# Optimization experiments

Measured on AMD Instinct MI355X. Metric: run time of the kernel, lower is better.

Reference implementation:

```python
import jax, jax.numpy as jnp
import numpy as np

N, E, F, ED, L = 50000, 800000, 64, 16, 2
EPS_BN = 1e-5


def setup_inputs() -> dict:
    key = jax.random.key(0)
    ks = jax.random.split(key, 8)
    s = 0.05
    return {
        "x": jax.random.normal(ks[0], (N, F), jnp.float32),
        "edge_index": jax.random.randint(ks[1], (2, E), 0, N),
        "edge_attr": jax.random.normal(ks[2], (E, ED), jnp.float32),
        # per-layer stacked params (L layers)
        "We": jax.random.normal(ks[3], (L, ED, F), jnp.float32) * s,
        "be": jnp.zeros((L, F), jnp.float32),
        "Wpre": jax.random.normal(ks[4], (L, 2 * F, F), jnp.float32) * s,
        "bpre": jnp.zeros((L, F), jnp.float32),
        "Wpost": jax.random.normal(ks[5], (L, 7 * F, F), jnp.float32) * s,
        "bpost": jnp.zeros((L, F), jnp.float32),
        "Wlin": jax.random.normal(ks[6], (L, F, F), jnp.float32) * s,
        "blin": jnp.zeros((L, F), jnp.float32),
        "gamma": jnp.ones((L, F), jnp.float32),
        "beta": jnp.zeros((L, F), jnp.float32),
    }


def _layer(x, src, dst, edge_attr, We, be, Wpre, bpre, Wpost, bpost, Wlin, blin, gamma, beta):
    # message: edge encoder + pre-MLP on cat(x_j, e)   [E, F]
    e = edge_attr @ We + be
    h = jnp.concatenate([x[src], e], axis=-1) @ Wpre + bpre
    # multi-aggregator segment reduce to target nodes (index = dst)
    cnt = jax.ops.segment_sum(jnp.ones(h.shape[0], h.dtype), dst, num_segments=N)
    safe_cnt = jnp.maximum(cnt, 1.0)
    mean = jax.ops.segment_sum(h, dst, num_segments=N) / safe_cnt[:, None]
    empty = (cnt == 0)[:, None]
    mn = jnp.where(empty, 0.0, jax.ops.segment_min(h, dst, num_segments=N))
    mx = jnp.where(empty, 0.0, jax.ops.segment_max(h, dst, num_segments=N))
    agg = jnp.concatenate([mean, mn, mx], axis=-1)  # [N, 3F]
    # scalers: identity, then amplification (deg=None => avg from bincount of degrees)
    deg_i = cnt.astype(jnp.int32)
    bc = jnp.bincount(deg_i, length=N).astype(h.dtype)
    avg_log = jnp.mean(jnp.log(bc + 1.0))
    amp = (jnp.log(safe_cnt + 1.0) / avg_log)[:, None]
    out = jnp.concatenate([agg, agg * amp], axis=-1)  # [N, 6F]
    # post-MLP on cat(x, aggregated), final linear
    out = jnp.concatenate([x, out], axis=-1) @ Wpost + bpost  # [N, F]
    out = out @ Wlin + blin
    # BatchNorm1d (batch stats, biased var) + ReLU
    mu = out.mean(axis=0)
    var = jnp.mean((out - mu) ** 2, axis=0)
    out = gamma * (out - mu) / jnp.sqrt(var + EPS_BN) + beta
    return jax.nn.relu(out)


def reference(x, edge_index, edge_attr, We, be, Wpre, bpre, Wpost, bpost, Wlin, blin, gamma, beta):
    src, dst = edge_index[0], edge_index[1]
    for l in range(L):
        x = _layer(x, src, dst, edge_attr, We[l], be[l], Wpre[l], bpre[l],
                   Wpost[l], bpost[l], Wlin[l], blin[l], gamma[l], beta[l])
    return x
```

## Files before the change

### kernel.cpp

```cpp
#include <hip/hip_runtime.h>
#include <math.h>

static constexpr int NN = 50000;
static constexpr long NE = 800000;
static constexpr int FF = 64;
static constexpr int EDIM = 16;
static constexpr int NLAYER = 2;
static constexpr float EPSBN = 1e-5f;
static constexpr int NGRP = NN / 16;
static constexpr int SCB = 512;
static constexpr int NSCB = (NN + SCB - 1) / SCB;
static constexpr int LDSW = 68;

typedef __attribute__((ext_vector_type(8))) short short8v;
typedef __attribute__((ext_vector_type(4))) float f32x4;

#define MFMA16(a, b, c) __builtin_amdgcn_mfma_f32_16x16x32_bf16(a, b, c, 0, 0, 0)

__device__ __forceinline__ short f2bf(float f) {
    unsigned u = __float_as_uint(f);
    unsigned r = u + 0x7FFFu + ((u >> 16) & 1u);
    return (short)(r >> 16);
}
__device__ __forceinline__ float bf2f(unsigned short h) {
    return __uint_as_float(((unsigned)h) << 16);
}
__device__ __forceinline__ unsigned pk2(float lo, float hi) {
    return (unsigned)(unsigned short)f2bf(lo) | ((unsigned)(unsigned short)f2bf(hi) << 16);
}
__device__ __forceinline__ short8v pack8(const float* p) {
    const float4* q = (const float4*)p;
    float4 a = q[0], b = q[1];
    short8v v;
    v[0] = f2bf(a.x); v[1] = f2bf(a.y); v[2] = f2bf(a.z); v[3] = f2bf(a.w);
    v[4] = f2bf(b.x); v[5] = f2bf(b.y); v[6] = f2bf(b.z); v[7] = f2bf(b.w);
    return v;
}
__device__ __forceinline__ void pack8s(const float* p, short8v& hi, short8v& lo) {
    const float4* q = (const float4*)p;
    float4 a = q[0], b = q[1];
    float v[8] = {a.x, a.y, a.z, a.w, b.x, b.y, b.z, b.w};
#pragma unroll
    for (int j = 0; j < 8; ++j) {
        short h = f2bf(v[j]);
        hi[j] = h;
        lo[j] = f2bf(v[j] - bf2f((unsigned short)h));
    }
}
__device__ __forceinline__ void pack8fs(const float* v, short8v& hi, short8v& lo) {
#pragma unroll
    for (int j = 0; j < 8; ++j) {
        short h = f2bf(v[j]);
        hi[j] = h;
        lo[j] = f2bf(v[j] - bf2f((unsigned short)h));
    }
}

__global__ void fold_kernel(const float* __restrict__ We, const float* __restrict__ be,
                            const float* __restrict__ Wpre, const float* __restrict__ bpre,
                            const float* __restrict__ Wpost, const float* __restrict__ bpost,
                            const float* __restrict__ Wlin, const float* __restrict__ blin,
                            float* __restrict__ Weff, float* __restrict__ beff,
                            float* __restrict__ Wc, float* __restrict__ cfold) {
    int l = blockIdx.x >> 4;
    int s = blockIdx.x & 15;
    int t = threadIdx.x;
    const float* We_l    = We    + l * EDIM * FF;
    const float* Wpre_e  = Wpre  + l * 2 * FF * FF + FF * FF;
    const float* Wpost_l = Wpost + l * 7 * FF * FF;
    const float* Wlin_l  = Wlin  + l * FF * FF;

    __shared__ float slin[FF * FF];
    __shared__ float spre[FF * FF];
    for (int i = t; i < FF * FF; i += blockDim.x) { slin[i] = Wlin_l[i]; spre[i] = Wpre_e[i]; }
    __syncthreads();

    for (int i = s * 256 + t; i < EDIM * FF; i += 16 * 256) {
        int j = i >> 6, f = i & 63;
        float a = 0.f;
        for (int k = 0; k < FF; ++k) a += We_l[j * FF + k] * spre[k * FF + f];
        Weff[l * EDIM * FF + i] = a;
    }
    for (int i = s * 256 + t; i < FF; i += 16 * 256) {
        float a = bpre[l * FF + i];
        for (int k = 0; k < FF; ++k) a += be[l * FF + k] * spre[k * FF + i];
        beff[l * FF + i] = a;
    }
    for (int i = s * 256 + t; i < 7 * FF * FF; i += 16 * 256) {
        int r = i >> 6, f = i & 63;
        float a = 0.f;
        for (int k = 0; k < FF; ++k) a += Wpost_l[r * FF + k] * slin[k * FF + f];
        Wc[l * 7 * FF * FF + i] = a;
    }
    for (int i = s * 256 + t; i < FF; i += 16 * 256) {
        float a = blin[l * FF + i];
        for (int k = 0; k < FF; ++k) a += bpost[l * FF + k] * slin[k * FF + i];
        cfold[l * FF + i] = a;
    }
}

__global__ void fragify_all(const float* __restrict__ Wpre, const float* __restrict__ Weff,
                            const float* __restrict__ Wc,
                            short* __restrict__ WpreF, short* __restrict__ WeffF,
                            short* __restrict__ WcFh, short* __restrict__ WcFl) {
    int b = blockIdx.x;
    int l = b / 17, r = b % 17;
    int t = threadIdx.x;
    const float* src; short* dh; short* dl = nullptr; int kc, Kreal;
    if (r < 2)      { src = Wpre + (size_t)l * 2 * FF * FF; dh = WpreF + l * 4096;  kc = r;     Kreal = 64; }
    else if (r < 3) { src = Weff + (size_t)l * EDIM * FF;   dh = WeffF + l * 2048;  kc = 0;     Kreal = 16; }
    else            { src = Wc   + (size_t)l * 7 * FF * FF; dh = WcFh + l * 28672;
                      dl = WcFl + l * 28672;                                        kc = r - 3; Kreal = 448; }
    int idx = kc * 256 + t;
    int lane = idx & 63, nt = (idx >> 6) & 3;
    int m = lane & 15, kh = lane >> 4;
    short8v hv, lv;
#pragma unroll
    for (int j = 0; j < 8; ++j) {
        int k = kc * 32 + kh * 8 + j;
        float val = (k < Kreal) ? src[k * FF + nt * 16 + m] : 0.f;
        short h = f2bf(val);
        hv[j] = h;
        lv[j] = f2bf(val - bf2f((unsigned short)h));
    }
    ((short8v*)dh)[idx] = hv;
    if (dl) ((short8v*)dl)[idx] = lv;
}


__global__ void build_zero(int* __restrict__ rowcnt, int* __restrict__ fill,
                           int* __restrict__ bc, float* __restrict__ avglog) {
    long i = (long)blockIdx.x * 256 + threadIdx.x;
    long stride = (long)gridDim.x * 256;
    for (long j = i; j < NN; j += stride) { rowcnt[j] = 0; fill[j] = 0; bc[j] = 0; }
    if (i == 0) avglog[0] = 0.f;
}

__global__ void hist_dst(const int* __restrict__ ei, int* __restrict__ rowcnt) {
    long e = (long)blockIdx.x * 256 + threadIdx.x;
    if (e < NE) atomicAdd(&rowcnt[ei[NE + e]], 1);
}

__global__ void scan_a(const int* __restrict__ rowcnt, int* __restrict__ part) {
    __shared__ int red[SCB];
    int t = threadIdx.x;
    int i = blockIdx.x * SCB + t;
    red[t] = (i < NN) ? rowcnt[i] : 0;
    __syncthreads();
    for (int o = SCB / 2; o > 0; o >>= 1) {
        if (t < o) red[t] += red[t + o];
        __syncthreads();
    }
    if (t == 0) part[blockIdx.x] = red[0];
}

__global__ void scan_b(int* __restrict__ part, int* __restrict__ rowptr) {
    __shared__ int s[128];
    int t = threadIdx.x;
    int v = (t < NSCB) ? part[t] : 0;
    s[t] = v;
    __syncthreads();
    for (int o = 1; o < 128; o <<= 1) {
        int u = (t >= o) ? s[t - o] : 0;
        __syncthreads();
        s[t] += u;
        __syncthreads();
    }
    if (t < NSCB) part[t] = s[t] - v;
    if (t == 127) rowptr[NN] = s[127];
}

__global__ void scan_c(const int* __restrict__ rowcnt, const int* __restrict__ part,
                       int* __restrict__ rowptr) {
    __shared__ int s[SCB];
    int t = threadIdx.x;
    int i = blockIdx.x * SCB + t;
    int v = (i < NN) ? rowcnt[i] : 0;
    s[t] = v;
    __syncthreads();
    for (int o = 1; o < SCB; o <<= 1) {
        int u = (t >= o) ? s[t - o] : 0;
        __syncthreads();
        s[t] += u;
        __syncthreads();
    }
    if (i < NN) rowptr[i] = part[blockIdx.x] + s[t] - v;
}

__global__ void scatter_perm(const int* __restrict__ ei, const int* __restrict__ rowptr,
                             int* __restrict__ fill, int2* __restrict__ srcperm) {
    long e = (long)blockIdx.x * 256 + threadIdx.x;
    if (e >= NE) return;
    int d = ei[NE + e];
    int p = rowptr[d] + atomicAdd(&fill[d], 1);
    srcperm[p] = make_int2(ei[e], (int)e);
}

__global__ void gather_attr(const int2* __restrict__ srcperm, const float* __restrict__ attr,
                            int* __restrict__ srcp, short* __restrict__ attrb) {
    long p = (long)blockIdx.x * 256 + threadIdx.x;
    if (p >= NE) return;
    int2 sp = srcperm[p];
    srcp[p] = sp.x;
    long e = sp.y;
    const float4* a4 = (const float4*)(attr + e * EDIM);
    float4 A = a4[0], B = a4[1], C = a4[2], D = a4[3];
    uint4 w0, w1;
    w0.x = pk2(A.x, A.y); w0.y = pk2(A.z, A.w); w0.z = pk2(B.x, B.y); w0.w = pk2(B.z, B.w);
    w1.x = pk2(C.x, C.y); w1.y = pk2(C.z, C.w); w1.z = pk2(D.x, D.y); w1.w = pk2(D.z, D.w);
    uint4* dst = (uint4*)(attrb + p * EDIM);
    dst[0] = w0; dst[1] = w1;
}

__global__ void degbc2(const int* __restrict__ rowcnt, int* __restrict__ bc) {
    __shared__ int h[256];
    int t = threadIdx.x;
    h[t] = 0;
    __syncthreads();
    for (long n = (long)blockIdx.x * 256 + t; n < NN; n += (long)gridDim.x * 256) {
        int d = rowcnt[n];
        if (d < 256) {
            atomicAdd(&h[d], 1);
        } else {
            if (d >= NN) d = NN - 1;
            atomicAdd(&bc[d], 1);
        }
    }
    __syncthreads();
    int v = h[t];
    if (v) atomicAdd(&bc[t], v);
}

__global__ void avglog_kernel(const int* __restrict__ bc, float* __restrict__ total) {
    float s = 0.f;
    for (long i = (long)blockIdx.x * 256 + threadIdx.x; i < NN; i += (long)gridDim.x * 256)
        s += logf((float)bc[i] + 1.f);
    for (int o = 32; o; o >>= 1) s += __shfl_down(s, o, 64);
    __shared__ float wsum[4];
    int lane = threadIdx.x & 63, wid = threadIdx.x >> 6;
    if (lane == 0) wsum[wid] = s;
    __syncthreads();
    if (threadIdx.x == 0) atomicAdd(total, wsum[0] + wsum[1] + wsum[2] + wsum[3]);
}

__global__ void amp_kernel(const int* __restrict__ cnt, const float* __restrict__ total,
                           float* __restrict__ amp) {
    long n = (long)blockIdx.x * 256 + threadIdx.x;
    if (n < NN) {
        float avg = total[0] / (float)NN;
        float sc = fmaxf((float)cnt[n], 1.f);
        amp[n] = logf(sc + 1.f) / avg;
    }
}


__global__ __launch_bounds__(256) void xp_mfma(const float* __restrict__ xin,
                                               const short* __restrict__ WF,
                                               short* __restrict__ xpb,
                                               float* __restrict__ bnsum,
                                               float* __restrict__ bnsum2) {
    int t = threadIdx.x;
    if (blockIdx.x == 0 && t < FF) { bnsum[t] = 0.f; bnsum2[t] = 0.f; }
    int g = blockIdx.x * 4 + (t >> 6);
    if (g >= NGRP) return;
    int lane = t & 63, m = lane & 15, kh = lane >> 4;
    const float* xr = xin + (long)(g * 16 + m) * FF;
    short8v a0 = pack8(xr + kh * 8);
    short8v a1 = pack8(xr + 32 + kh * 8);
    const short8v* BF = (const short8v*)WF;
    f32x4 acc[4];
#pragma unroll
    for (int nt = 0; nt < 4; ++nt) {
        f32x4 z = {0.f, 0.f, 0.f, 0.f};
        z = MFMA16(a0, BF[(0 * 4 + nt) * 64 + lane], z);
        z = MFMA16(a1, BF[(1 * 4 + nt) * 64 + lane], z);
        acc[nt] = z;
    }
#pragma unroll
    for (int nt = 0; nt < 4; ++nt)
#pragma unroll
        for (int r = 0; r < 4; ++r) {
            long node = g * 16 + kh * 4 + r;
            xpb[node * FF + nt * 16 + m] = f2bf(acc[nt][r]);
        }
}

__global__ __launch_bounds__(256) void agg_fused(
    const int* __restrict__ rowptr, const int* __restrict__ srcp,
    const short* __restrict__ attrb, const short* __restrict__ WF,
    const float* __restrict__ beff_l, const short* __restrict__ xpb,
    float* __restrict__ sumb, float* __restrict__ mnb, float* __restrict__ mxb) {
    __shared__ float eph[4][16 * LDSW];
    int t = threadIdx.x;
    int wid = t >> 6, lane = t & 63;
    int m = lane & 15, kh = lane >> 4;
    int n = blockIdx.x * 4 + wid;
    if (n >= NN) return;
    float* lds = &eph[wid][0];
    const short8v* BF = (const short8v*)WF;
    float bfv[4];
#pragma unroll
    for (int nt = 0; nt < 4; ++nt) bfv[nt] = beff_l[nt * 16 + m];
    long r0 = rowptr[n], r1 = rowptr[n + 1];
    const float INF = __builtin_huge_valf();
    float sm = 0.f, mn = INF, mx = -INF;
    const unsigned short* xu = (const unsigned short*)xpb;

    for (long base = r0; base < r1; base += 16) {
        int cnt = (int)(((r1 - base) < 16) ? (r1 - base) : 16);
        long ea = base + m; if (ea > NE - 1) ea = NE - 1;
        short8v a;
        if (kh < 2) {
            a = *(const short8v*)(attrb + ea * EDIM + kh * 8);
        } else {
#pragma unroll
            for (int j = 0; j < 8; ++j) a[j] = 0;
        }
        f32x4 ac0, ac1, ac2, ac3;
        {
            f32x4 z = {0.f, 0.f, 0.f, 0.f};
            ac0 = MFMA16(a, BF[0 * 64 + lane], z);
            ac1 = MFMA16(a, BF[1 * 64 + lane], z);
            ac2 = MFMA16(a, BF[2 * 64 + lane], z);
            ac3 = MFMA16(a, BF[3 * 64 + lane], z);
        }
#pragma unroll
        for (int r = 0; r < 4; ++r) {
            lds[(kh * 4 + r) * LDSW + 0 * 16 + m] = ac0[r] + bfv[0];
            lds[(kh * 4 + r) * LDSW + 1 * 16 + m] = ac1[r] + bfv[1];
            lds[(kh * 4 + r) * LDSW + 2 * 16 + m] = ac2[r] + bfv[2];
            lds[(kh * 4 + r) * LDSW + 3 * 16 + m] = ac3[r] + bfv[3];
        }
        int sv = srcp[base + (lane < cnt ? lane : cnt - 1)];
        int j = 0;
        for (; j + 8 <= cnt; j += 8) {
            int s0 = __shfl(sv, j + 0), s1 = __shfl(sv, j + 1);
            int s2 = __shfl(sv, j + 2), s3 = __shfl(sv, j + 3);
            int s4 = __shfl(sv, j + 4), s5 = __shfl(sv, j + 5);
            int s6 = __shfl(sv, j + 6), s7 = __shfl(sv, j + 7);
            float x0 = bf2f(xu[(long)s0 * FF + lane]);
            float x1 = bf2f(xu[(long)s1 * FF + lane]);
            float x2 = bf2f(xu[(long)s2 * FF + lane]);
            float x3 = bf2f(xu[(long)s3 * FF + lane]);
            float x4 = bf2f(xu[(long)s4 * FF + lane]);
            float x5 = bf2f(xu[(long)s5 * FF + lane]);
            float x6 = bf2f(xu[(long)s6 * FF + lane]);
            float x7 = bf2f(xu[(long)s7 * FF + lane]);
            float h0 = x0 + lds[(j + 0) * LDSW + lane];
            float h1 = x1 + lds[(j + 1) * LDSW + lane];
            float h2 = x2 + lds[(j + 2) * LDSW + lane];
            float h3 = x3 + lds[(j + 3) * LDSW + lane];
            float h4 = x4 + lds[(j + 4) * LDSW + lane];
            float h5 = x5 + lds[(j + 5) * LDSW + lane];
            float h6 = x6 + lds[(j + 6) * LDSW + lane];
            float h7 = x7 + lds[(j + 7) * LDSW + lane];
            sm += ((h0 + h1) + (h2 + h3)) + ((h4 + h5) + (h6 + h7));
            mn = fminf(mn, fminf(fminf(fminf(h0, h1), fminf(h2, h3)),
                                 fminf(fminf(h4, h5), fminf(h6, h7))));
            mx = fmaxf(mx, fmaxf(fmaxf(fmaxf(h0, h1), fmaxf(h2, h3)),
                                 fmaxf(fmaxf(h4, h5), fmaxf(h6, h7))));
        }
        for (; j < cnt; ++j) {
            int s0 = __shfl(sv, j);
            float h = bf2f(xu[(long)s0 * FF + lane]) + lds[j * LDSW + lane];
            sm += h;
            mn = fminf(mn, h);
            mx = fmaxf(mx, h);
        }
    }
    long o = (long)n * FF + lane;
    sumb[o] = sm; mnb[o] = mn; mxb[o] = mx;
}

__global__ __launch_bounds__(256) void node_mfma(
    const float* __restrict__ xin, const float* __restrict__ sumb,
    const float* __restrict__ mnb, const float* __restrict__ mxb,
    const int* __restrict__ rowcnt, const float* __restrict__ amp,
    const short* __restrict__ WFh, const short* __restrict__ WFl,
    const float* __restrict__ cfold_l,
    float* __restrict__ out_pre, float* __restrict__ bnsum, float* __restrict__ bnsum2) {
    __shared__ float sS[FF], sQ[FF];
    int t = threadIdx.x;
    if (t < FF) { sS[t] = 0.f; sQ[t] = 0.f; }
    __syncthreads();
    int g = blockIdx.x * 4 + (t >> 6);
    bool act = (g < NGRP);
    int lane = t & 63, m = lane & 15, kh = lane >> 4;
    if (act) {
        long n = g * 16 + m;
        int deg = rowcnt[n];
        float inv = 1.f / fmaxf((float)deg, 1.f);
        bool has = (deg > 0);
        float av = amp[n];
        const float* xr = xin + n * FF;
        float vme[16], vmn[16], vmx[16], sc16[16];
        {
            const float4* s4a = (const float4*)(sumb + n * FF + kh * 8);
            const float4* s4b = (const float4*)(sumb + n * FF + 32 + kh * 8);
            float4 a = s4a[0], b = s4a[1], c = s4b[0], d = s4b[1];
            vme[0]=a.x*inv; vme[1]=a.y*inv; vme[2]=a.z*inv; vme[3]=a.w*inv;
            vme[4]=b.x*inv; vme[5]=b.y*inv; vme[6]=b.z*inv; vme[7]=b.w*inv;
            vme[8]=c.x*inv; vme[9]=c.y*inv; vme[10]=c.z*inv; vme[11]=c.w*inv;
            vme[12]=d.x*inv; vme[13]=d.y*inv; vme[14]=d.z*inv; vme[15]=d.w*inv;
        }
        {
            const float4* s4a = (const float4*)(mnb + n * FF + kh * 8);
            const float4* s4b = (const float4*)(mnb + n * FF + 32 + kh * 8);
            float4 a = s4a[0], b = s4a[1], c = s4b[0], d = s4b[1];
            vmn[0]=has?a.x:0.f; vmn[1]=has?a.y:0.f; vmn[2]=has?a.z:0.f; vmn[3]=has?a.w:0.f;
            vmn[4]=has?b.x:0.f; vmn[5]=has?b.y:0.f; vmn[6]=has?b.z:0.f; vmn[7]=has?b.w:0.f;
            vmn[8]=has?c.x:0.f; vmn[9]=has?c.y:0.f; vmn[10]=has?c.z:0.f; vmn[11]=has?c.w:0.f;
            vmn[12]=has?d.x:0.f; vmn[13]=has?d.y:0.f; vmn[14]=has?d.z:0.f; vmn[15]=has?d.w:0.f;
        }
        {
            const float4* s4a = (const float4*)(mxb + n * FF + kh * 8);
            const float4* s4b = (const float4*)(mxb + n * FF + 32 + kh * 8);
            float4 a = s4a[0], b = s4a[1], c = s4b[0], d = s4b[1];
            vmx[0]=has?a.x:0.f; vmx[1]=has?a.y:0.f; vmx[2]=has?a.z:0.f; vmx[3]=has?a.w:0.f;
            vmx[4]=has?b.x:0.f; vmx[5]=has?b.y:0.f; vmx[6]=has?b.z:0.f; vmx[7]=has?b.w:0.f;
            vmx[8]=has?c.x:0.f; vmx[9]=has?c.y:0.f; vmx[10]=has?c.z:0.f; vmx[11]=has?c.w:0.f;
            vmx[12]=has?d.x:0.f; vmx[13]=has?d.y:0.f; vmx[14]=has?d.z:0.f; vmx[15]=has?d.w:0.f;
        }
        const short8v* BH = (const short8v*)WFh;
        const short8v* BL = (const short8v*)WFl;
        f32x4 acc[4];
#pragma unroll
        for (int nt = 0; nt < 4; ++nt) { f32x4 z = {0.f,0.f,0.f,0.f}; acc[nt] = z; }
        short8v hv, lv;
#define DO_KC3(kc) { \
        _Pragma("unroll") for (int nt = 0; nt < 4; ++nt) { \
            acc[nt] = MFMA16(hv, BH[((kc) * 4 + nt) * 64 + lane], acc[nt]); \
            acc[nt] = MFMA16(lv, BH[((kc) * 4 + nt) * 64 + lane], acc[nt]); \
            acc[nt] = MFMA16(hv, BL[((kc) * 4 + nt) * 64 + lane], acc[nt]); } }
        pack8s(xr + kh * 8, hv, lv);        DO_KC3(0)
        pack8s(xr + 32 + kh * 8, hv, lv);   DO_KC3(1)
        pack8fs(vme + 0, hv, lv);           DO_KC3(2)
        pack8fs(vme + 8, hv, lv);           DO_KC3(3)
        pack8fs(vmn + 0, hv, lv);           DO_KC3(4)
        pack8fs(vmn + 8, hv, lv);           DO_KC3(5)
        pack8fs(vmx + 0, hv, lv);           DO_KC3(6)
        pack8fs(vmx + 8, hv, lv);           DO_KC3(7)
#pragma unroll
        for (int j = 0; j < 16; ++j) sc16[j] = vme[j] * av;
        pack8fs(sc16 + 0, hv, lv);          DO_KC3(8)
        pack8fs(sc16 + 8, hv, lv);          DO_KC3(9)
#pragma unroll
        for (int j = 0; j < 16; ++j) sc16[j] = vmn[j] * av;
        pack8fs(sc16 + 0, hv, lv);          DO_KC3(10)
        pack8fs(sc16 + 8, hv, lv);          DO_KC3(11)
#pragma unroll
        for (int j = 0; j < 16; ++j) sc16[j] = vmx[j] * av;
        pack8fs(sc16 + 0, hv, lv);          DO_KC3(12)
        pack8fs(sc16 + 8, hv, lv);          DO_KC3(13)
#undef DO_KC3
        float cfv[4];
#pragma unroll
        for (int nt = 0; nt < 4; ++nt) cfv[nt] = cfold_l[nt * 16 + m];
#pragma unroll
        for (int nt = 0; nt < 4; ++nt) {
            float ps = 0.f, pq = 0.f;
#pragma unroll
            for (int r = 0; r < 4; ++r) {
                float v = acc[nt][r] + cfv[nt];
                out_pre[(long)(g * 16 + kh * 4 + r) * FF + nt * 16 + m] = v;
                ps += v;
                pq += v * v;
            }
            atomicAdd(&sS[nt * 16 + m], ps);
            atomicAdd(&sQ[nt * 16 + m], pq);
        }
    }
    __syncthreads();
    if (t < FF) {
        atomicAdd(&bnsum[t], sS[t]);
        atomicAdd(&bnsum2[t], sQ[t]);
    }
}

__global__ void bn_apply2(const float* __restrict__ out_pre,
                          const float* __restrict__ bnsum, const float* __restrict__ bnsum2,
                          const float* __restrict__ gamma_l, const float* __restrict__ beta_l,
                          float* __restrict__ xout) {
    int f = threadIdx.x & 63;
    float mu = bnsum[f] / (float)NN;
    float var = bnsum2[f] / (float)NN - mu * mu;
    var = fmaxf(var, 0.f);
    float s = gamma_l[f] * rsqrtf(var + EPSBN);
    float o = beta_l[f] - mu * s;
    long i = (long)blockIdx.x * 256 + threadIdx.x;
    long stride = (long)gridDim.x * 256;
    for (long j = i; j < (long)NN * FF; j += stride) {
        xout[j] = fmaxf(fmaf(out_pre[j], s, o), 0.f);
    }
}

extern "C" void kernel_launch(void* const* d_in, const int* in_sizes, int n_in,
                              void* d_out, int out_size, void* d_ws, size_t ws_size,
                              hipStream_t stream) {
    const float* x0    = (const float*)d_in[0];
    const int*   ei    = (const int*)d_in[1];
    const float* attr  = (const float*)d_in[2];
    const float* We    = (const float*)d_in[3];
    const float* be    = (const float*)d_in[4];
    const float* Wpre  = (const float*)d_in[5];
    const float* bpre  = (const float*)d_in[6];
    const float* Wpost = (const float*)d_in[7];
    const float* bpost = (const float*)d_in[8];
    const float* Wlin  = (const float*)d_in[9];
    const float* blin  = (const float*)d_in[10];
    const float* gamma = (const float*)d_in[11];
    const float* beta  = (const float*)d_in[12];
    float* out = (float*)d_out;

    char* ws = (char*)d_ws;
    size_t off = 0;
    auto carve = [&](size_t bytes) -> void* {
        void* p = ws + off;
        off += (bytes + 255) & ~(size_t)255;
        return p;
    };
    const size_t NFb = (size_t)NN * FF * 4;
    float*    Weff   = (float*)carve(2 * EDIM * FF * 4);
    float*    beff   = (float*)carve(2 * FF * 4);
    float*    Wc     = (float*)carve(2 * 7 * FF * FF * 4);
    float*    cfold  = (float*)carve(2 * FF * 4);
    short*    WpreF  = (short*)carve(2 * 4096 * 2);
    short*    WeffF  = (short*)carve(2 * 2048 * 2);
    short*    WcFh   = (short*)carve(2 * 28672 * 2);
    short*    WcFl   = (short*)carve(2 * 28672 * 2);
    int*      srcp   = (int*)carve(NE * 4);
    short*    attrb  = (short*)carve((size_t)NE * EDIM * 2);
    int*      rowptr = (int*)carve((NN + 1) * 4);
    int*      rowcnt = (int*)carve(NN * 4);
    int*      fill   = (int*)carve(NN * 4);
    int*      bc     = (int*)carve(NN * 4);
    float*    amp    = (float*)carve(NN * 4);
    int*      part   = (int*)carve(NSCB * 4);
    short*    xpb    = (short*)carve((size_t)NN * FF * 2);
    float*    sumb   = (float*)carve(NFb);
    float*    mnb    = (float*)carve(NFb);
    float*    mxb    = (float*)carve(NFb);
    float*    xbuf   = (float*)carve(NFb);
    float*    out_pre = (float*)carve(NFb);
    float*    bnsum  = (float*)carve(FF * 4);
    float*    bnsum2 = (float*)carve(FF * 4);
    float*    avglog = (float*)carve(4);
    int2*     srcperm = (int2*)xbuf;

    const int EB = (int)((NE + 255) / 256);

    build_zero<<<196, 256, 0, stream>>>(rowcnt, fill, bc, avglog);
    hist_dst<<<EB, 256, 0, stream>>>(ei, rowcnt);
    scan_a<<<NSCB, SCB, 0, stream>>>(rowcnt, part);
    scan_b<<<1, 128, 0, stream>>>(part, rowptr);
    scan_c<<<NSCB, SCB, 0, stream>>>(rowcnt, part, rowptr);
    scatter_perm<<<EB, 256, 0, stream>>>(ei, rowptr, fill, srcperm);
    gather_attr<<<EB, 256, 0, stream>>>(srcperm, attr, srcp, attrb);
    degbc2<<<196, 256, 0, stream>>>(rowcnt, bc);
    avglog_kernel<<<128, 256, 0, stream>>>(bc, avglog);
    amp_kernel<<<196, 256, 0, stream>>>(rowcnt, avglog, amp);
    fold_kernel<<<32, 256, 0, stream>>>(We, be, Wpre, bpre, Wpost, bpost, Wlin, blin,
                                        Weff, beff, Wc, cfold);
    fragify_all<<<34, 256, 0, stream>>>(Wpre, Weff, Wc, WpreF, WeffF, WcFh, WcFl);

    for (int l = 0; l < NLAYER; ++l) {
        const float* xin = (l == 0) ? x0 : xbuf;
        float* xout = (l == NLAYER - 1) ? out : xbuf;

        xp_mfma<<<(NGRP + 3) / 4, 256, 0, stream>>>(xin, WpreF + l * 4096, xpb, bnsum, bnsum2);
        agg_fused<<<12500, 256, 0, stream>>>(rowptr, srcp, attrb, WeffF + l * 2048,
                                             beff + l * FF, xpb, sumb, mnb, mxb);
        node_mfma<<<(NGRP + 3) / 4, 256, 0, stream>>>(xin, sumb, mnb, mxb, rowcnt, amp,
                                                      WcFh + l * 28672, WcFl + l * 28672,
                                                      cfold + l * FF,
                                                      out_pre, bnsum, bnsum2);
        bn_apply2<<<4096, 256, 0, stream>>>(out_pre, bnsum, bnsum2,
                                            gamma + l * FF, beta + l * FF, xout);
    }
}
```

Baseline: 348.5 us.

## Fuse BatchNorm+ReLU of inner layer into next layer's input loads

For every layer except the last, the separate BN-apply pass is replaced by a tiny kernel that computes per-feature scale and shift. The next layer's xp_mfma and node_mfma apply scale, shift and ReLU while loading the raw pre-activations. This removes a full N×F read and write pass per inner layer, but the affine transform is now computed twice, once in each consumer. The diff also moves mean division and empty-node zeroing into agg_fused, splits the node_mfma accumulators into two independent chains, and adds a launch_bounds occupancy hint.

```diff
diff --git a/kernel.cpp b/kernel.cpp
--- a/kernel.cpp
+++ b/kernel.cpp
@@ -36,6 +36,18 @@
     v[4] = f2bf(b.x); v[5] = f2bf(b.y); v[6] = f2bf(b.z); v[7] = f2bf(b.w);
     return v;
 }
+__device__ __forceinline__ short8v pack8bn(const float* p, const float* sc, int f0) {
+    const float4* q = (const float4*)p;
+    float4 a = q[0], b = q[1];
+    float v[8] = {a.x, a.y, a.z, a.w, b.x, b.y, b.z, b.w};
+    short8v r;
+#pragma unroll
+    for (int j = 0; j < 8; ++j) {
+        float y = fmaxf(fmaf(v[j], sc[f0 + j], sc[FF + f0 + j]), 0.f);
+        r[j] = f2bf(y);
+    }
+    return r;
+}
 __device__ __forceinline__ void pack8s(const float* p, short8v& hi, short8v& lo) {
     const float4* q = (const float4*)p;
     float4 a = q[0], b = q[1];
@@ -45,6 +57,19 @@
         short h = f2bf(v[j]);
         hi[j] = h;
         lo[j] = f2bf(v[j] - bf2f((unsigned short)h));
+    }
+}
+__device__ __forceinline__ void pack8s_bn(const float* p, const float* sc, int f0,
+                                          short8v& hi, short8v& lo) {
+    const float4* q = (const float4*)p;
+    float4 a = q[0], b = q[1];
+    float v[8] = {a.x, a.y, a.z, a.w, b.x, b.y, b.z, b.w};
+#pragma unroll
+    for (int j = 0; j < 8; ++j) {
+        float y = fmaxf(fmaf(v[j], sc[f0 + j], sc[FF + f0 + j]), 0.f);
+        short h = f2bf(y);
+        hi[j] = h;
+        lo[j] = f2bf(y - bf2f((unsigned short)h));
     }
 }
 __device__ __forceinline__ void pack8fs(const float* v, short8v& hi, short8v& lo) {
@@ -255,6 +280,7 @@
 
 
 __global__ __launch_bounds__(256) void xp_mfma(const float* __restrict__ xin,
+                                               const float* __restrict__ bnsc,
                                                const short* __restrict__ WF,
                                                short* __restrict__ xpb,
                                                float* __restrict__ bnsum,
@@ -265,8 +291,14 @@
     if (g >= NGRP) return;
     int lane = t & 63, m = lane & 15, kh = lane >> 4;
     const float* xr = xin + (long)(g * 16 + m) * FF;
-    short8v a0 = pack8(xr + kh * 8);
-    short8v a1 = pack8(xr + 32 + kh * 8);
+    short8v a0, a1;
+    if (bnsc) {
+        a0 = pack8bn(xr + kh * 8, bnsc, kh * 8);
+        a1 = pack8bn(xr + 32 + kh * 8, bnsc, 32 + kh * 8);
+    } else {
+        a0 = pack8(xr + kh * 8);
+        a1 = pack8(xr + 32 + kh * 8);
+    }
     const short8v* BF = (const short8v*)WF;
     f32x4 acc[4];
 #pragma unroll
@@ -289,7 +321,7 @@
     const int* __restrict__ rowptr, const int* __restrict__ srcp,
     const short* __restrict__ attrb, const short* __restrict__ WF,
     const float* __restrict__ beff_l, const short* __restrict__ xpb,
-    float* __restrict__ sumb, float* __restrict__ mnb, float* __restrict__ mxb) {
+    float* __restrict__ meanb, float* __restrict__ mnb, float* __restrict__ mxb) {
     __shared__ float eph[4][16 * LDSW];
     int t = threadIdx.x;
     int wid = t >> 6, lane = t & 63;
@@ -368,14 +400,17 @@
             mx = fmaxf(mx, h);
         }
     }
+    int deg = (int)(r1 - r0);
+    float inv = (deg > 0) ? (1.f / (float)deg) : 0.f;
+    if (deg == 0) { mn = 0.f; mx = 0.f; }
     long o = (long)n * FF + lane;
-    sumb[o] = sm; mnb[o] = mn; mxb[o] = mx;
-}
-
-__global__ __launch_bounds__(256) void node_mfma(
-    const float* __restrict__ xin, const float* __restrict__ sumb,
-    const float* __restrict__ mnb, const float* __restrict__ mxb,
-    const int* __restrict__ rowcnt, const float* __restrict__ amp,
+    meanb[o] = sm * inv; mnb[o] = mn; mxb[o] = mx;
+}
+
+__global__ __launch_bounds__(256, 2) void node_mfma(
+    const float* __restrict__ xin, const float* __restrict__ bnsc,
+    const float* __restrict__ meanb, const float* __restrict__ mnb,
+    const float* __restrict__ mxb, const float* __restrict__ amp,
     const short* __restrict__ WFh, const short* __restrict__ WFl,
     const float* __restrict__ cfold_l,
     float* __restrict__ out_pre, float* __restrict__ bnsum, float* __restrict__ bnsum2) {
@@ -388,70 +423,75 @@
     int lane = t & 63, m = lane & 15, kh = lane >> 4;
     if (act) {
         long n = g * 16 + m;
-        int deg = rowcnt[n];
-        float inv = 1.f / fmaxf((float)deg, 1.f);
-        bool has = (deg > 0);
         float av = amp[n];
         const float* xr = xin + n * FF;
         float vme[16], vmn[16], vmx[16], sc16[16];
         {
-            const float4* s4a = (const float4*)(sumb + n * FF + kh * 8);
-            const float4* s4b = (const float4*)(sumb + n * FF + 32 + kh * 8);
+            const float4* s4a = (const float4*)(meanb + n * FF + kh * 8);
+            const float4* s4b = (const float4*)(meanb + n * FF + 32 + kh * 8);
             float4 a = s4a[0], b = s4a[1], c = s4b[0], d = s4b[1];
-            vme[0]=a.x*inv; vme[1]=a.y*inv; vme[2]=a.z*inv; vme[3]=a.w*inv;
-            vme[4]=b.x*inv; vme[5]=b.y*inv; vme[6]=b.z*inv; vme[7]=b.w*inv;
-            vme[8]=c.x*inv; vme[9]=c.y*inv; vme[10]=c.z*inv; vme[11]=c.w*inv;
-            vme[12]=d.x*inv; vme[13]=d.y*inv; vme[14]=d.z*inv; vme[15]=d.w*inv;
+            vme[0]=a.x; vme[1]=a.y; vme[2]=a.z; vme[3]=a.w;
+            vme[4]=b.x; vme[5]=b.y; vme[6]=b.z; vme[7]=b.w;
+            vme[8]=c.x; vme[9]=c.y; vme[10]=c.z; vme[11]=c.w;
+            vme[12]=d.x; vme[13]=d.y; vme[14]=d.z; vme[15]=d.w;
         }
         {
             const float4* s4a = (const float4*)(mnb + n * FF + kh * 8);
             const float4* s4b = (const float4*)(mnb + n * FF + 32 + kh * 8);
             float4 a = s4a[0], b = s4a[1], c = s4b[0], d = s4b[1];
-            vmn[0]=has?a.x:0.f; vmn[1]=has?a.y:0.f; vmn[2]=has?a.z:0.f; vmn[3]=has?a.w:0.f;
-            vmn[4]=has?b.x:0.f; vmn[5]=has?b.y:0.f; vmn[6]=has?b.z:0.f; vmn[7]=has?b.w:0.f;
-            vmn[8]=has?c.x:0.f; vmn[9]=has?c.y:0.f; vmn[10]=has?c.z:0.f; vmn[11]=has?c.w:0.f;
-            vmn[12]=has?d.x:0.f; vmn[13]=has?d.y:0.f; vmn[14]=has?d.z:0.f; vmn[15]=has?d.w:0.f;
+            vmn[0]=a.x; vmn[1]=a.y; vmn[2]=a.z; vmn[3]=a.w;
+            vmn[4]=b.x; vmn[5]=b.y; vmn[6]=b.z; vmn[7]=b.w;
+            vmn[8]=c.x; vmn[9]=c.y; vmn[10]=c.z; vmn[11]=c.w;
+            vmn[12]=d.x; vmn[13]=d.y; vmn[14]=d.z; vmn[15]=d.w;
         }
         {
             const float4* s4a = (const float4*)(mxb + n * FF + kh * 8);
             const float4* s4b = (const float4*)(mxb + n * FF + 32 + kh * 8);
             float4 a = s4a[0], b = s4a[1], c = s4b[0], d = s4b[1];
-            vmx[0]=has?a.x:0.f; vmx[1]=has?a.y:0.f; vmx[2]=has?a.z:0.f; vmx[3]=has?a.w:0.f;
-            vmx[4]=has?b.x:0.f; vmx[5]=has?b.y:0.f; vmx[6]=has?b.z:0.f; vmx[7]=has?b.w:0.f;
-            vmx[8]=has?c.x:0.f; vmx[9]=has?c.y:0.f; vmx[10]=has?c.z:0.f; vmx[11]=has?c.w:0.f;
-            vmx[12]=has?d.x:0.f; vmx[13]=has?d.y:0.f; vmx[14]=has?d.z:0.f; vmx[15]=has?d.w:0.f;
+            vmx[0]=a.x; vmx[1]=a.y; vmx[2]=a.z; vmx[3]=a.w;
+            vmx[4]=b.x; vmx[5]=b.y; vmx[6]=b.z; vmx[7]=b.w;
+            vmx[8]=c.x; vmx[9]=c.y; vmx[10]=c.z; vmx[11]=c.w;
+            vmx[12]=d.x; vmx[13]=d.y; vmx[14]=d.z; vmx[15]=d.w;
         }
         const short8v* BH = (const short8v*)WFh;
         const short8v* BL = (const short8v*)WFl;
-        f32x4 acc[4];
-#pragma unroll
-        for (int nt = 0; nt < 4; ++nt) { f32x4 z = {0.f,0.f,0.f,0.f}; acc[nt] = z; }
+        f32x4 accA[4], accB[4];
+#pragma unroll
+        for (int nt = 0; nt < 4; ++nt) {
+            f32x4 z = {0.f, 0.f, 0.f, 0.f};
+            accA[nt] = z; accB[nt] = z;
+        }
         short8v hv, lv;
-#define DO_KC3(kc) { \
+#define DO_KC3(kc, ACC) { \
         _Pragma("unroll") for (int nt = 0; nt < 4; ++nt) { \
-            acc[nt] = MFMA16(hv, BH[((kc) * 4 + nt) * 64 + lane], acc[nt]); \
-            acc[nt] = MFMA16(lv, BH[((kc) * 4 + nt) * 64 + lane], acc[nt]); \
-            acc[nt] = MFMA16(hv, BL[((kc) * 4 + nt) * 64 + lane], acc[nt]); } }
-        pack8s(xr + kh * 8, hv, lv);        DO_KC3(0)
-        pack8s(xr + 32 + kh * 8, hv, lv);   DO_KC3(1)
-        pack8fs(vme + 0, hv, lv);           DO_KC3(2)
-        pack8fs(vme + 8, hv, lv);           DO_KC3(3)
-        pack8fs(vmn + 0, hv, lv);           DO_KC3(4)
-        pack8fs(vmn + 8, hv, lv);           DO_KC3(5)
-        pack8fs(vmx + 0, hv, lv);           DO_KC3(6)
-        pack8fs(vmx + 8, hv, lv);           DO_KC3(7)
+            ACC[nt] = MFMA16(hv, BH[((kc) * 4 + nt) * 64 + lane], ACC[nt]); \
+            ACC[nt] = MFMA16(lv, BH[((kc) * 4 + nt) * 64 + lane], ACC[nt]); \
+            ACC[nt] = MFMA16(hv, BL[((kc) * 4 + nt) * 64 + lane], ACC[nt]); } }
+        if (bnsc) {
+            pack8s_bn(xr + kh * 8, bnsc, kh * 8, hv, lv);           DO_KC3(0, accA)
+            pack8s_bn(xr + 32 + kh * 8, bnsc, 32 + kh * 8, hv, lv); DO_KC3(1, accB)
+        } else {
+            pack8s(xr + kh * 8, hv, lv);        DO_KC3(0, accA)
+            pack8s(xr + 32 + kh * 8, hv, lv);   DO_KC3(1, accB)
+        }
+        pack8fs(vme + 0, hv, lv);           DO_KC3(2, accA)
+        pack8fs(vme + 8, hv, lv);           DO_KC3(3, accB)
+        pack8fs(vmn + 0, hv, lv);           DO_KC3(4, accA)
+        pack8fs(vmn + 8, hv, lv);           DO_KC3(5, accB)
+        pack8fs(vmx + 0, hv, lv);           DO_KC3(6, accA)
+        pack8fs(vmx + 8, hv, lv);           DO_KC3(7, accB)
 #pragma unroll
         for (int j = 0; j < 16; ++j) sc16[j] = vme[j] * av;
-        pack8fs(sc16 + 0, hv, lv);          DO_KC3(8)
-        pack8fs(sc16 + 8, hv, lv);          DO_KC3(9)
+        pack8fs(sc16 + 0, hv, lv);          DO_KC3(8, accA)
+        pack8fs(sc16 + 8, hv, lv);          DO_KC3(9, accB)
 #pragma unroll
         for (int j = 0; j < 16; ++j) sc16[j] = vmn[j] * av;
-        pack8fs(sc16 + 0, hv, lv);          DO_KC3(10)
-        pack8fs(sc16 + 8, hv, lv);          DO_KC3(11)
+        pack8fs(sc16 + 0, hv, lv);          DO_KC3(10, accA)
+        pack8fs(sc16 + 8, hv, lv);          DO_KC3(11, accB)
 #pragma unroll
         for (int j = 0; j < 16; ++j) sc16[j] = vmx[j] * av;
-        pack8fs(sc16 + 0, hv, lv);          DO_KC3(12)
-        pack8fs(sc16 + 8, hv, lv);          DO_KC3(13)
+        pack8fs(sc16 + 0, hv, lv);          DO_KC3(12, accA)
+        pack8fs(sc16 + 8, hv, lv);          DO_KC3(13, accB)
 #undef DO_KC3
         float cfv[4];
 #pragma unroll
@@ -461,7 +501,7 @@
             float ps = 0.f, pq = 0.f;
 #pragma unroll
             for (int r = 0; r < 4; ++r) {
-                float v = acc[nt][r] + cfv[nt];
+                float v = accA[nt][r] + accB[nt][r] + cfv[nt];
                 out_pre[(long)(g * 16 + kh * 4 + r) * FF + nt * 16 + m] = v;
                 ps += v;
                 pq += v * v;
@@ -474,6 +514,20 @@
     if (t < FF) {
         atomicAdd(&bnsum[t], sS[t]);
         atomicAdd(&bnsum2[t], sQ[t]);
+    }
+}
+
+__global__ void bn_final(const float* __restrict__ bnsum, const float* __restrict__ bnsum2,
+                         const float* __restrict__ gamma_l, const float* __restrict__ beta_l,
+                         float* __restrict__ sc_sh) {
+    int f = threadIdx.x;
+    if (f < FF) {
+        float mu = bnsum[f] / (float)NN;
+        float var = bnsum2[f] / (float)NN - mu * mu;
+        var = fmaxf(var, 0.f);
+        float s = gamma_l[f] * rsqrtf(var + EPSBN);
+        sc_sh[f] = s;
+        sc_sh[FF + f] = beta_l[f] - mu * s;
     }
 }
 
@@ -537,15 +591,16 @@
     float*    amp    = (float*)carve(NN * 4);
     int*      part   = (int*)carve(NSCB * 4);
     short*    xpb    = (short*)carve((size_t)NN * FF * 2);
-    float*    sumb   = (float*)carve(NFb);
+    float*    meanb  = (float*)carve(NFb);
     float*    mnb    = (float*)carve(NFb);
     float*    mxb    = (float*)carve(NFb);
-    float*    xbuf   = (float*)carve(NFb);
-    float*    out_pre = (float*)carve(NFb);
+    float*    preA   = (float*)carve(NFb);
+    float*    preB   = (float*)carve(NFb);
     float*    bnsum  = (float*)carve(FF * 4);
     float*    bnsum2 = (float*)carve(FF * 4);
     float*    avglog = (float*)carve(4);
-    int2*     srcperm = (int2*)xbuf;
+    float*    sc_sh  = (float*)carve(2 * FF * 4);
+    int2*     srcperm = (int2*)preB;
 
     const int EB = (int)((NE + 255) / 256);
 
@@ -564,17 +619,22 @@
     fragify_all<<<34, 256, 0, stream>>>(Wpre, Weff, Wc, WpreF, WeffF, WcFh, WcFl);
 
     for (int l = 0; l < NLAYER; ++l) {
-        const float* xin = (l == 0) ? x0 : xbuf;
-        float* xout = (l == NLAYER - 1) ? out : xbuf;
-
-        xp_mfma<<<(NGRP + 3) / 4, 256, 0, stream>>>(xin, WpreF + l * 4096, xpb, bnsum, bnsum2);
+        const float* xin  = (l == 0) ? x0 : ((l & 1) ? preA : preB);
+        const float* bnsc = (l == 0) ? nullptr : sc_sh;
+        float* pre        = (l & 1) ? preB : preA;
+
+        xp_mfma<<<(NGRP + 3) / 4, 256, 0, stream>>>(xin, bnsc, WpreF + l * 4096, xpb,
+                                                    bnsum, bnsum2);
         agg_fused<<<12500, 256, 0, stream>>>(rowptr, srcp, attrb, WeffF + l * 2048,
-                                             beff + l * FF, xpb, sumb, mnb, mxb);
-        node_mfma<<<(NGRP + 3) / 4, 256, 0, stream>>>(xin, sumb, mnb, mxb, rowcnt, amp,
+                                             beff + l * FF, xpb, meanb, mnb, mxb);
+        node_mfma<<<(NGRP + 3) / 4, 256, 0, stream>>>(xin, bnsc, meanb, mnb, mxb, amp,
                                                       WcFh + l * 28672, WcFl + l * 28672,
                                                       cfold + l * FF,
-                                                      out_pre, bnsum, bnsum2);
-        bn_apply2<<<4096, 256, 0, stream>>>(out_pre, bnsum, bnsum2,
-                                            gamma + l * FF, beta + l * FF, xout);
-    }
-}
+                                                      pre, bnsum, bnsum2);
+        if (l < NLAYER - 1)
+            bn_final<<<1, 64, 0, stream>>>(bnsum, bnsum2, gamma + l * FF, beta + l * FF, sc_sh);
+        else
+            bn_apply2<<<4096, 256, 0, stream>>>(pre, bnsum, bnsum2,
+                                                gamma + l * FF, beta + l * FF, out);
+    }
+}
```

Result: no change. 353.6 us (+1.5%).
